# Kernel tuning notes

Hardware: AMD Instinct MI355X
Metric: run time of the kernel (lower is better)

The kernel has to match this reference:

```python
import jax, jax.numpy as jnp
import numpy as np

N_NODES = 100000


def _graph_conv(x, src, dst, W, b):
    # DGL GraphConv, norm='both':
    # out = D_in^{-1/2} A D_out^{-1/2} x W + b, degrees clamped >= 1
    ones = jnp.ones(src.shape[0], dtype=x.dtype)
    deg_out = jax.ops.segment_sum(ones, src, num_segments=N_NODES)
    deg_in = jax.ops.segment_sum(ones, dst, num_segments=N_NODES)
    norm_src = jax.lax.rsqrt(jnp.maximum(deg_out, 1.0))  # [N]
    norm_dst = jax.lax.rsqrt(jnp.maximum(deg_in, 1.0))   # [N]
    h = x * norm_src[:, None]                    # [N, d_in]
    msg = h[src]                                 # [E, d_in] gather
    agg = jax.ops.segment_sum(msg, dst, num_segments=N_NODES)  # [N, d_in] scatter-add
    agg = agg * norm_dst[:, None]
    return agg @ W + b                           # [N, d_out]


def setup_inputs() -> dict:
    key = jax.random.key(0)
    k1, k2, k3, k4, k5 = jax.random.split(key, 5)
    n_edges = 1600000
    ndim, hdl, r = 32, 64, 32
    x = jax.random.normal(k1, (N_NODES, ndim), dtype=jnp.float32)
    src = jax.random.randint(k2, (n_edges,), 0, N_NODES, dtype=jnp.int32)
    dst = jax.random.randint(k3, (n_edges,), 0, N_NODES, dtype=jnp.int32)
    W1 = jax.random.normal(k4, (ndim, hdl), dtype=jnp.float32) / np.sqrt(ndim)
    b1 = jnp.zeros((hdl,), dtype=jnp.float32)
    W2 = jax.random.normal(k5, (hdl, r), dtype=jnp.float32) / np.sqrt(hdl)
    b2 = jnp.zeros((r,), dtype=jnp.float32)
    return {"x": x, "src": src, "dst": dst, "W1": W1, "b1": b1, "W2": W2, "b2": b2}


def reference(x, src, dst, W1, b1, W2, b2):
    z = _graph_conv(x, src, dst, W1, b1)
    z = _graph_conv(z, src, dst, W2, b2)
    return z
```

## Files before the change

### kernel.cpp

```cpp
#include <hip/hip_runtime.h>

#define N_NODES 100000
#define D_IN 32
#define D_HID 64
#define D_OUT 32
#define NBUCK 391
#define CHUNK 8192
#define CAP   8192

typedef unsigned short ushort8v __attribute__((ext_vector_type(8)));
typedef unsigned short ushort4v __attribute__((ext_vector_type(4)));

__device__ __forceinline__ float bf2f(unsigned short u) {
    return __uint_as_float((unsigned)u << 16);
}
__device__ __forceinline__ unsigned short f2bf(float f) {
    unsigned u = __float_as_uint(f);
    return (unsigned short)((u + 0x7FFF + ((u >> 16) & 1)) >> 16);
}

#define REDH(a) { a += __shfl_xor(a, 4); a += __shfl_xor(a, 8); a += __shfl_xor(a, 16); }

__global__ __launch_bounds__(256) void bucket_hist_kernel(
    const int* __restrict__ src, const int* __restrict__ dst,
    int* __restrict__ sb_cnt, int* __restrict__ db_cnt, int E) {
    __shared__ int hs[NBUCK], hd[NBUCK];
    int tid = threadIdx.x;
    for (int i = tid; i < NBUCK; i += 256) { hs[i] = 0; hd[i] = 0; }
    __syncthreads();
    int stride = gridDim.x * 256;
    for (int e = blockIdx.x * 256 + tid; e < E; e += stride) {
        atomicAdd(&hs[src[e] >> 8], 1);
        atomicAdd(&hd[dst[e] >> 8], 1);
    }
    __syncthreads();
    for (int i = tid; i < NBUCK; i += 256) {
        if (hs[i]) atomicAdd(&sb_cnt[i], hs[i]);
        if (hd[i]) atomicAdd(&db_cnt[i], hd[i]);
    }
}

__global__ __launch_bounds__(512) void bucket_scan_kernel(
    const int* __restrict__ sb_cnt, const int* __restrict__ db_cnt,
    int* __restrict__ sb_base, int* __restrict__ db_base,
    int* __restrict__ sb_cur, int* __restrict__ db_cur, int E) {
    __shared__ int s[512];
    int tid = threadIdx.x;
    int v = (tid < NBUCK) ? sb_cnt[tid] : 0;
    s[tid] = v;
    __syncthreads();
    for (int off = 1; off < 512; off <<= 1) {
        int tv = (tid >= off) ? s[tid - off] : 0;
        __syncthreads(); s[tid] += tv; __syncthreads();
    }
    if (tid < NBUCK) { int e0 = s[tid] - v; sb_base[tid] = e0; sb_cur[tid] = e0; }
    if (tid == 0) sb_base[NBUCK] = E;
    __syncthreads();
    int v2 = (tid < NBUCK) ? db_cnt[tid] : 0;
    s[tid] = v2;
    __syncthreads();
    for (int off = 1; off < 512; off <<= 1) {
        int tv = (tid >= off) ? s[tid - off] : 0;
        __syncthreads(); s[tid] += tv; __syncthreads();
    }
    if (tid < NBUCK) { int e0 = s[tid] - v2; db_base[tid] = e0; db_cur[tid] = e0; }
    if (tid == 0) db_base[NBUCK] = E;
}

__global__ __launch_bounds__(512) void partition_both_kernel(
    const int* __restrict__ src, const int* __restrict__ dst,
    int* __restrict__ sb_cur, int* __restrict__ db_cur,
    int* __restrict__ ebuf, unsigned char* __restrict__ sbuf, int E) {
    __shared__ int dh[NBUCK], sh_[NBUCK];
    __shared__ int sarr[512];
    __shared__ int dloff[NBUCK], dgb[NBUCK], dcur[NBUCK];
    __shared__ int sloff[NBUCK], sgb[NBUCK], scur[NBUCK];
    __shared__ int dbuf[CHUNK];
    __shared__ unsigned char sbytes[CHUNK];
    int tid = threadIdx.x;
    int base = blockIdx.x * CHUNK;
    int lim = E - base; if (lim > CHUNK) lim = CHUNK;

    for (int i = tid; i < NBUCK; i += 512) { dh[i] = 0; sh_[i] = 0; }
    __syncthreads();
    for (int k = tid; k < lim; k += 512) {
        atomicAdd(&dh[dst[base + k] >> 8], 1);
        atomicAdd(&sh_[src[base + k] >> 8], 1);
    }
    __syncthreads();
    int v = (tid < NBUCK) ? dh[tid] : 0;
    sarr[tid] = v;
    __syncthreads();
    for (int off = 1; off < 512; off <<= 1) {
        int tv = (tid >= off) ? sarr[tid - off] : 0;
        __syncthreads(); sarr[tid] += tv; __syncthreads();
    }
    if (tid < NBUCK) {
        int excl = sarr[tid] - v;
        dloff[tid] = excl; dcur[tid] = excl;
        dgb[tid] = v ? atomicAdd(&db_cur[tid], v) : 0;
    }
    __syncthreads();
    int v2 = (tid < NBUCK) ? sh_[tid] : 0;
    sarr[tid] = v2;
    __syncthreads();
    for (int off = 1; off < 512; off <<= 1) {
        int tv = (tid >= off) ? sarr[tid - off] : 0;
        __syncthreads(); sarr[tid] += tv; __syncthreads();
    }
    if (tid < NBUCK) {
        int excl = sarr[tid] - v2;
        sloff[tid] = excl; scur[tid] = excl;
        sgb[tid] = v2 ? atomicAdd(&sb_cur[tid], v2) : 0;
    }
    __syncthreads();
    for (int k = tid; k < lim; k += 512) {
        int d = dst[base + k], s0 = src[base + k];
        int p = atomicAdd(&dcur[d >> 8], 1);
        dbuf[p] = (s0 << 8) | (d & 255);
        int p2 = atomicAdd(&scur[s0 >> 8], 1);
        sbytes[p2] = (unsigned char)(s0 & 255);
    }
    __syncthreads();
    int w = tid >> 6, lane = tid & 63;
    for (int b = w; b < NBUCK; b += 8) {
        int st = dloff[b], len = dh[b], gb = dgb[b];
        for (int i = lane; i < len; i += 64) ebuf[gb + i] = dbuf[st + i];
        int st2 = sloff[b], len2 = sh_[b], gb2 = sgb[b];
        for (int i = lane; i < len2; i += 64) sbuf[gb2 + i] = sbytes[st2 + i];
    }
}

__global__ __launch_bounds__(256) void src_norm_prescale_kernel(
    const unsigned char* __restrict__ sbuf, const int* __restrict__ sb_base,
    const float4* __restrict__ x4, ushort4v* __restrict__ xs4b,
    float* __restrict__ norm_src, int n_nodes) {
    __shared__ int cnt[256];
    __shared__ float nsl[256];
    int b = blockIdx.x, tid = threadIdx.x;
    int st = sb_base[b], en = sb_base[b + 1];
    cnt[tid] = 0;
    __syncthreads();
    for (int k = st + tid; k < en; k += 256) atomicAdd(&cnt[sbuf[k]], 1);
    __syncthreads();
    int base_node = b << 8;
    int nn = n_nodes - base_node; if (nn > 256) nn = 256;
    if (tid < nn) {
        int d = cnt[tid];
        float ns = rsqrtf((float)(d < 1 ? 1 : d));
        norm_src[base_node + tid] = ns;
        nsl[tid] = ns;
    }
    __syncthreads();
    for (int k = tid; k < nn * 8; k += 256) {
        float4 v = x4[((long)base_node << 3) + k];
        float s = nsl[k >> 3];
        ushort4v o;
        o[0] = f2bf(v.x * s); o[1] = f2bf(v.y * s);
        o[2] = f2bf(v.z * s); o[3] = f2bf(v.w * s);
        xs4b[((long)base_node << 3) + k] = o;
    }
}

__global__ __launch_bounds__(256) void localfill_kernel(
    const int* __restrict__ ebuf, const int* __restrict__ db_base,
    int* __restrict__ rowptr, float* __restrict__ norm_dst,
    int* __restrict__ colidx, int n_nodes, int E) {
    __shared__ int limg[CAP];
    __shared__ int cnt[256];
    __shared__ int sc[256];
    int b = blockIdx.x, tid = threadIdx.x;
    int base_node = b << 8;
    int nn = n_nodes - base_node; if (nn > 256) nn = 256;
    int cbase = db_base[b], cend = db_base[b + 1];
    int len = cend - cbase;
    cnt[tid] = 0;
    __syncthreads();
    for (int k = tid; k < len; k += 256) atomicAdd(&cnt[ebuf[cbase + k] & 255], 1);
    __syncthreads();
    int v = cnt[tid];
    sc[tid] = v;
    __syncthreads();
    for (int off = 1; off < 256; off <<= 1) {
        int tv = (tid >= off) ? sc[tid - off] : 0;
        __syncthreads(); sc[tid] += tv; __syncthreads();
    }
    int excl = sc[tid] - v;
    if (tid < nn) {
        rowptr[base_node + tid] = cbase + excl;
        norm_dst[base_node + tid] = rsqrtf((float)(v < 1 ? 1 : v));
    }
    if (b == NBUCK - 1 && tid == 0) rowptr[n_nodes] = E;
    __syncthreads();
    cnt[tid] = excl;
    __syncthreads();
    if (len <= CAP) {
        for (int k = tid; k < len; k += 256) {
            int v2 = ebuf[cbase + k];
            int p = atomicAdd(&cnt[v2 & 255], 1);
            limg[p] = v2 >> 8;
        }
        __syncthreads();
        for (int k = tid; k < len; k += 256) colidx[cbase + k] = limg[k];
    } else {
        for (int k = tid; k < len; k += 256) {
            int v2 = ebuf[cbase + k];
            int p = atomicAdd(&cnt[v2 & 255], 1);
            colidx[cbase + p] = v2 >> 8;
        }
    }
}

__global__ __launch_bounds__(256) void gather1_kernel(
    const ushort8v* __restrict__ xs8, const int* __restrict__ colidx,
    const int* __restrict__ rowptr, float* __restrict__ agg, int n_nodes) {
    int t = threadIdx.x;
    int w = t >> 6, lane = t & 63;
    int half = lane >> 5, hl = lane & 31;
    int eh = hl >> 2, q = hl & 3;
    int hb = half << 5;
    int npairs = (n_nodes + 1) >> 1;

    for (int p = blockIdx.x * 4 + w; p < npairs; p += gridDim.x * 4) {
        int nA = 2 * p, nB = nA + 1;
        bool hasB = nB < n_nodes;
        int rA = rowptr[nA], rA1 = rowptr[nA + 1];
        int rB1 = hasB ? rowptr[nB + 1] : rA1;
        int dA = rA1 - rA, dB = rB1 - rA1;
        int dmax = dA > dB ? dA : dB;
        int myS = half ? rA1 : rA;
        int myD = half ? dB : dA;
        float a[8];
#pragma unroll
        for (int r = 0; r < 8; ++r) a[r] = 0.f;
        for (int base = 0; base < dmax; base += 32) {
            int mylim = myD - base; mylim = mylim < 0 ? 0 : (mylim > 32 ? 32 : mylim);
            int c_reg = (hl < mylim) ? colidx[myS + base + hl] : 0;
            int c0 = __shfl(c_reg, hb | eh);
            int c1 = __shfl(c_reg, hb | (eh + 8));
            int c2 = __shfl(c_reg, hb | (eh + 16));
            int c3 = __shfl(c_reg, hb | (eh + 24));
            ushort8v v0 = xs8[(long)c0 * 4 + q];
            ushort8v v1 = xs8[(long)c1 * 4 + q];
            ushort8v v2 = xs8[(long)c2 * 4 + q];
            ushort8v v3 = xs8[(long)c3 * 4 + q];
            float m0 = (eh      < mylim) ? 1.f : 0.f;
            float m1 = (eh +  8 < mylim) ? 1.f : 0.f;
            float m2 = (eh + 16 < mylim) ? 1.f : 0.f;
            float m3 = (eh + 24 < mylim) ? 1.f : 0.f;
#pragma unroll
            for (int r = 0; r < 8; ++r) {
                a[r] = fmaf(bf2f(v0[r]), m0, a[r]);
                a[r] = fmaf(bf2f(v1[r]), m1, a[r]);
                a[r] = fmaf(bf2f(v2[r]), m2, a[r]);
                a[r] = fmaf(bf2f(v3[r]), m3, a[r]);
            }
        }
#pragma unroll
        for (int r = 0; r < 8; ++r) REDH(a[r])
        if (hl < 4) {
            int n_ = half ? nB : nA;
            if (!half || hasB) {
                float* orow = agg + (long)n_ * 32 + q * 8;
                float4 o1, o2;
                o1.x = a[0]; o1.y = a[1]; o1.z = a[2]; o1.w = a[3];
                o2.x = a[4]; o2.y = a[5]; o2.z = a[6]; o2.w = a[7];
                ((float4*)orow)[0] = o1;
                ((float4*)orow)[1] = o2;
            }
        }
    }
}

__global__ __launch_bounds__(256) void gemm_fused_kernel(
    const float* __restrict__ agg, const float* __restrict__ norm_src,
    const float* __restrict__ norm_dst,
    const float* __restrict__ W1, const float* __restrict__ b1,
    const float* __restrict__ W2, unsigned short* __restrict__ ybf, int n_nodes) {
    __shared__ float W1s[D_IN * D_HID];
    __shared__ float W2s[D_HID * D_OUT];
    __shared__ float b1s[D_HID];
    __shared__ float accs[4][2][D_IN];
    __shared__ float z1s[4][2][D_HID];
    int t = threadIdx.x;
    for (int i = t; i < 2048; i += 256) { W1s[i] = W1[i]; W2s[i] = W2[i]; }
    if (t < D_HID) b1s[t] = b1[t];
    __syncthreads();
    int w = t >> 6, lane = t & 63;
    int half = lane >> 5, hl = lane & 31;
    int npairs = (n_nodes + 1) >> 1;
    for (int p = blockIdx.x * 4 + w; p < npairs; p += gridDim.x * 4) {
        int nA = 2 * p, nB = nA + 1;
        bool hasB = nB < n_nodes;
        int nh = half ? (hasB ? nB : nA) : nA;
        accs[w][half][hl] = agg[(long)nh * 32 + hl];
        float ndA = norm_dst[nA], ndB = hasB ? norm_dst[nB] : 0.f;
        float s1A = 0.f, s1B = 0.f;
#pragma unroll
        for (int k = 0; k < D_IN; ++k) {
            float wv = W1s[k * D_HID + lane];
            s1A = fmaf(accs[w][0][k], wv, s1A);
            s1B = fmaf(accs[w][1][k], wv, s1B);
        }
        z1s[w][0][lane] = ndA * s1A + b1s[lane];
        z1s[w][1][lane] = ndB * s1B + b1s[lane];
        float s2 = 0.f;
#pragma unroll
        for (int k = 0; k < D_HID; ++k) s2 = fmaf(z1s[w][half][k], W2s[k * D_OUT + hl], s2);
        int n_ = half ? nB : nA;
        if (!half || hasB) ybf[(long)n_ * 32 + hl] = f2bf(norm_src[n_] * s2);
    }
}

__global__ __launch_bounds__(256) void gather2_kernel(
    const ushort8v* __restrict__ y8, const int* __restrict__ colidx,
    const int* __restrict__ rowptr, const float* __restrict__ norm_dst,
    const float* __restrict__ b2, float* __restrict__ out, int n_nodes) {
    int t = threadIdx.x;
    int w = t >> 6, lane = t & 63;
    int half = lane >> 5, hl = lane & 31;
    int eh = hl >> 2, q = hl & 3;
    int hb = half << 5;
    int npairs = (n_nodes + 1) >> 1;

    for (int p = blockIdx.x * 4 + w; p < npairs; p += gridDim.x * 4) {
        int nA = 2 * p, nB = nA + 1;
        bool hasB = nB < n_nodes;
        int rA = rowptr[nA], rA1 = rowptr[nA + 1];
        int rB1 = hasB ? rowptr[nB + 1] : rA1;
        int dA = rA1 - rA, dB = rB1 - rA1;
        int dmax = dA > dB ? dA : dB;
        int myS = half ? rA1 : rA;
        int myD = half ? dB : dA;
        float a[8];
#pragma unroll
        for (int r = 0; r < 8; ++r) a[r] = 0.f;
        for (int base = 0; base < dmax; base += 32) {
            int mylim = myD - base; mylim = mylim < 0 ? 0 : (mylim > 32 ? 32 : mylim);
            int c_reg = (hl < mylim) ? colidx[myS + base + hl] : 0;
            int c0 = __shfl(c_reg, hb | eh);
            int c1 = __shfl(c_reg, hb | (eh + 8));
            int c2 = __shfl(c_reg, hb | (eh + 16));
            int c3 = __shfl(c_reg, hb | (eh + 24));
            ushort8v v0 = y8[(long)c0 * 4 + q];
            ushort8v v1 = y8[(long)c1 * 4 + q];
            ushort8v v2 = y8[(long)c2 * 4 + q];
            ushort8v v3 = y8[(long)c3 * 4 + q];
            float m0 = (eh      < mylim) ? 1.f : 0.f;
            float m1 = (eh +  8 < mylim) ? 1.f : 0.f;
            float m2 = (eh + 16 < mylim) ? 1.f : 0.f;
            float m3 = (eh + 24 < mylim) ? 1.f : 0.f;
#pragma unroll
            for (int r = 0; r < 8; ++r) {
                a[r] = fmaf(bf2f(v0[r]), m0, a[r]);
                a[r] = fmaf(bf2f(v1[r]), m1, a[r]);
                a[r] = fmaf(bf2f(v2[r]), m2, a[r]);
                a[r] = fmaf(bf2f(v3[r]), m3, a[r]);
            }
        }
#pragma unroll
        for (int r = 0; r < 8; ++r) REDH(a[r])
        if (hl < 4) {
            int n_ = half ? nB : nA;
            if (!half || hasB) {
                float nd = norm_dst[n_];
                const float4 bL = ((const float4*)b2)[q * 2];
                const float4 bH = ((const float4*)b2)[q * 2 + 1];
                float4 o1, o2;
                o1.x = fmaf(a[0], nd, bL.x); o1.y = fmaf(a[1], nd, bL.y);
                o1.z = fmaf(a[2], nd, bL.z); o1.w = fmaf(a[3], nd, bL.w);
                o2.x = fmaf(a[4], nd, bH.x); o2.y = fmaf(a[5], nd, bH.y);
                o2.z = fmaf(a[6], nd, bH.z); o2.w = fmaf(a[7], nd, bH.w);
                float* orow = out + (long)n_ * 32 + q * 8;
                ((float4*)orow)[0] = o1;
                ((float4*)orow)[1] = o2;
            }
        }
    }
}

extern "C" void kernel_launch(void* const* d_in, const int* in_sizes, int n_in,
                              void* d_out, int out_size, void* d_ws, size_t ws_size,
                              hipStream_t stream) {
    const float* x   = (const float*)d_in[0];
    const int*   src = (const int*)d_in[1];
    const int*   dst = (const int*)d_in[2];
    const float* W1  = (const float*)d_in[3];
    const float* b1  = (const float*)d_in[4];
    const float* W2  = (const float*)d_in[5];
    const float* b2  = (const float*)d_in[6];

    const int N = N_NODES;
    const int E = in_sizes[1];

    int* ws_i    = (int*)d_ws;
    int* sb_cnt  = ws_i;
    int* db_cnt  = ws_i + 512;
    int* sb_base = ws_i + 1024;
    int* db_base = ws_i + 1536;
    int* sb_cur  = ws_i + 2048;
    int* db_cur  = ws_i + 2560;
    int* rowptr  = ws_i + 3072;
    int* colidx  = ws_i + 103104;
    float* norms = (float*)(ws_i + 1703104);
    int* ebuf    = ws_i + 1903104;
    unsigned char* sbuf = (unsigned char*)(ws_i + 3503104);
    unsigned short* xsb = (unsigned short*)(ws_i + 3903104);
    float* agg   = (float*)(ws_i + 5503104);
    unsigned short* ybf = (unsigned short*)ebuf;

    hipMemsetAsync(ws_i, 0, 1024 * sizeof(int), stream);

    bucket_hist_kernel<<<256, 256, 0, stream>>>(src, dst, sb_cnt, db_cnt, E);
    bucket_scan_kernel<<<1, 512, 0, stream>>>(sb_cnt, db_cnt, sb_base, db_base,
                                              sb_cur, db_cur, E);

    int pb = (E + CHUNK - 1) / CHUNK;
    partition_both_kernel<<<pb, 512, 0, stream>>>(src, dst, sb_cur, db_cur,
                                                  ebuf, sbuf, E);
    src_norm_prescale_kernel<<<NBUCK, 256, 0, stream>>>(sbuf, sb_base,
                                                        (const float4*)x, (ushort4v*)xsb,
                                                        norms, N);
    localfill_kernel<<<NBUCK, 256, 0, stream>>>(ebuf, db_base, rowptr, norms + N,
                                                colidx, N, E);

    gather1_kernel<<<2048, 256, 0, stream>>>((const ushort8v*)xsb, colidx, rowptr,
                                             agg, N);
    gemm_fused_kernel<<<2048, 256, 0, stream>>>(agg, norms, norms + N,
                                                W1, b1, W2, ybf, N);
    gather2_kernel<<<2048, 256, 0, stream>>>((const ushort8v*)ybf, colidx, rowptr,
                                             norms + N, b2, (float*)d_out, N);
}
```

Baseline: 175.0 us.

## Merge bucket finalize kernels, use quarter-wave per node in gathers, replace memset

The source-norm prescale and the CSR localfill kernels are merged into one per-bucket kernel, which removes a launch and its dependency gap. Both gather kernels now give each 16-lane quarter-wave one destination node instead of each 32-lane half-wave, so a wave processes four nodes. Average in-degree is about 16, so less of each wave sits idle on masked lanes. The memset is replaced by a tiny zeroing kernel to avoid memset API overhead. The merged kernel uses more shared memory per block, and the quarter-wave layout needs more loop iterations for high-degree nodes.

```diff
diff --git a/kernel.cpp b/kernel.cpp
--- a/kernel.cpp
+++ b/kernel.cpp
@@ -19,7 +19,9 @@
     return (unsigned short)((u + 0x7FFF + ((u >> 16) & 1)) >> 16);
 }
 
-#define REDH(a) { a += __shfl_xor(a, 4); a += __shfl_xor(a, 8); a += __shfl_xor(a, 16); }
+__global__ void zero_counts_kernel(int* __restrict__ p) {
+    p[blockIdx.x * 256 + threadIdx.x] = 0;
+}
 
 __global__ __launch_bounds__(256) void bucket_hist_kernel(
     const int* __restrict__ src, const int* __restrict__ dst,
@@ -131,20 +133,26 @@
     }
 }
 
-__global__ __launch_bounds__(256) void src_norm_prescale_kernel(
+__global__ __launch_bounds__(256) void bucket_finalize_kernel(
     const unsigned char* __restrict__ sbuf, const int* __restrict__ sb_base,
     const float4* __restrict__ x4, ushort4v* __restrict__ xs4b,
-    float* __restrict__ norm_src, int n_nodes) {
+    float* __restrict__ norm_src,
+    const int* __restrict__ ebuf, const int* __restrict__ db_base,
+    int* __restrict__ rowptr, float* __restrict__ norm_dst,
+    int* __restrict__ colidx, int n_nodes, int E) {
+    __shared__ int limg[CAP];
     __shared__ int cnt[256];
+    __shared__ int sc[256];
     __shared__ float nsl[256];
     int b = blockIdx.x, tid = threadIdx.x;
+    int base_node = b << 8;
+    int nn = n_nodes - base_node; if (nn > 256) nn = 256;
+
     int st = sb_base[b], en = sb_base[b + 1];
     cnt[tid] = 0;
     __syncthreads();
     for (int k = st + tid; k < en; k += 256) atomicAdd(&cnt[sbuf[k]], 1);
     __syncthreads();
-    int base_node = b << 8;
-    int nn = n_nodes - base_node; if (nn > 256) nn = 256;
     if (tid < nn) {
         int d = cnt[tid];
         float ns = rsqrtf((float)(d < 1 ? 1 : d));
@@ -160,20 +168,10 @@
         o[2] = f2bf(v.z * s); o[3] = f2bf(v.w * s);
         xs4b[((long)base_node << 3) + k] = o;
     }
-}
-
-__global__ __launch_bounds__(256) void localfill_kernel(
-    const int* __restrict__ ebuf, const int* __restrict__ db_base,
-    int* __restrict__ rowptr, float* __restrict__ norm_dst,
-    int* __restrict__ colidx, int n_nodes, int E) {
-    __shared__ int limg[CAP];
-    __shared__ int cnt[256];
-    __shared__ int sc[256];
-    int b = blockIdx.x, tid = threadIdx.x;
-    int base_node = b << 8;
-    int nn = n_nodes - base_node; if (nn > 256) nn = 256;
+
     int cbase = db_base[b], cend = db_base[b + 1];
     int len = cend - cbase;
+    __syncthreads();
     cnt[tid] = 0;
     __syncthreads();
     for (int k = tid; k < len; k += 256) atomicAdd(&cnt[ebuf[cbase + k] & 255], 1);
@@ -216,38 +214,40 @@
     const int* __restrict__ rowptr, float* __restrict__ agg, int n_nodes) {
     int t = threadIdx.x;
     int w = t >> 6, lane = t & 63;
-    int half = lane >> 5, hl = lane & 31;
-    int eh = hl >> 2, q = hl & 3;
-    int hb = half << 5;
-    int npairs = (n_nodes + 1) >> 1;
-
-    for (int p = blockIdx.x * 4 + w; p < npairs; p += gridDim.x * 4) {
-        int nA = 2 * p, nB = nA + 1;
-        bool hasB = nB < n_nodes;
-        int rA = rowptr[nA], rA1 = rowptr[nA + 1];
-        int rB1 = hasB ? rowptr[nB + 1] : rA1;
-        int dA = rA1 - rA, dB = rB1 - rA1;
-        int dmax = dA > dB ? dA : dB;
-        int myS = half ? rA1 : rA;
-        int myD = half ? dB : dA;
+    int quarter = lane >> 4, ql = lane & 15;
+    int eh = ql >> 2, q = ql & 3;
+    int qb = quarter << 4;
+    int nquads = (n_nodes + 3) >> 2;
+
+    for (int p = blockIdx.x * 4 + w; p < nquads; p += gridDim.x * 4) {
+        int base_node = p << 2;
+        int idx = base_node + lane;
+        if (idx > n_nodes) idx = n_nodes;
+        int rr = (lane < 5) ? rowptr[idx] : 0;
+        int myS = __shfl(rr, quarter);
+        int myE = __shfl(rr, quarter + 1);
+        int myD = myE - myS;
+        int dm = myD;
+        dm = max(dm, __shfl_xor(dm, 16));
+        dm = max(dm, __shfl_xor(dm, 32));
         float a[8];
 #pragma unroll
         for (int r = 0; r < 8; ++r) a[r] = 0.f;
-        for (int base = 0; base < dmax; base += 32) {
-            int mylim = myD - base; mylim = mylim < 0 ? 0 : (mylim > 32 ? 32 : mylim);
-            int c_reg = (hl < mylim) ? colidx[myS + base + hl] : 0;
-            int c0 = __shfl(c_reg, hb | eh);
-            int c1 = __shfl(c_reg, hb | (eh + 8));
-            int c2 = __shfl(c_reg, hb | (eh + 16));
-            int c3 = __shfl(c_reg, hb | (eh + 24));
+        for (int base = 0; base < dm; base += 16) {
+            int mylim = myD - base; mylim = mylim < 0 ? 0 : (mylim > 16 ? 16 : mylim);
+            int c_reg = (ql < mylim) ? colidx[myS + base + ql] : 0;
+            int c0 = __shfl(c_reg, qb | eh);
+            int c1 = __shfl(c_reg, qb | (eh + 4));
+            int c2 = __shfl(c_reg, qb | (eh + 8));
+            int c3 = __shfl(c_reg, qb | (eh + 12));
             ushort8v v0 = xs8[(long)c0 * 4 + q];
             ushort8v v1 = xs8[(long)c1 * 4 + q];
             ushort8v v2 = xs8[(long)c2 * 4 + q];
             ushort8v v3 = xs8[(long)c3 * 4 + q];
             float m0 = (eh      < mylim) ? 1.f : 0.f;
-            float m1 = (eh +  8 < mylim) ? 1.f : 0.f;
-            float m2 = (eh + 16 < mylim) ? 1.f : 0.f;
-            float m3 = (eh + 24 < mylim) ? 1.f : 0.f;
+            float m1 = (eh +  4 < mylim) ? 1.f : 0.f;
+            float m2 = (eh +  8 < mylim) ? 1.f : 0.f;
+            float m3 = (eh + 12 < mylim) ? 1.f : 0.f;
 #pragma unroll
             for (int r = 0; r < 8; ++r) {
                 a[r] = fmaf(bf2f(v0[r]), m0, a[r]);
@@ -257,11 +257,11 @@
             }
         }
 #pragma unroll
-        for (int r = 0; r < 8; ++r) REDH(a[r])
-        if (hl < 4) {
-            int n_ = half ? nB : nA;
-            if (!half || hasB) {
-                float* orow = agg + (long)n_ * 32 + q * 8;
+        for (int r = 0; r < 8; ++r) { a[r] += __shfl_xor(a[r], 4); a[r] += __shfl_xor(a[r], 8); }
+        if (ql < 4) {
+            int n_ = base_node + quarter;
+            if (n_ < n_nodes) {
+                float* orow = agg + (long)n_ * 32 + ql * 8;
                 float4 o1, o2;
                 o1.x = a[0]; o1.y = a[1]; o1.z = a[2]; o1.w = a[3];
                 o2.x = a[4]; o2.y = a[5]; o2.z = a[6]; o2.w = a[7];
@@ -318,38 +318,40 @@
     const float* __restrict__ b2, float* __restrict__ out, int n_nodes) {
     int t = threadIdx.x;
     int w = t >> 6, lane = t & 63;
-    int half = lane >> 5, hl = lane & 31;
-    int eh = hl >> 2, q = hl & 3;
-    int hb = half << 5;
-    int npairs = (n_nodes + 1) >> 1;
-
-    for (int p = blockIdx.x * 4 + w; p < npairs; p += gridDim.x * 4) {
-        int nA = 2 * p, nB = nA + 1;
-        bool hasB = nB < n_nodes;
-        int rA = rowptr[nA], rA1 = rowptr[nA + 1];
-        int rB1 = hasB ? rowptr[nB + 1] : rA1;
-        int dA = rA1 - rA, dB = rB1 - rA1;
-        int dmax = dA > dB ? dA : dB;
-        int myS = half ? rA1 : rA;
-        int myD = half ? dB : dA;
+    int quarter = lane >> 4, ql = lane & 15;
+    int eh = ql >> 2, q = ql & 3;
+    int qb = quarter << 4;
+    int nquads = (n_nodes + 3) >> 2;
+
+    for (int p = blockIdx.x * 4 + w; p < nquads; p += gridDim.x * 4) {
+        int base_node = p << 2;
+        int idx = base_node + lane;
+        if (idx > n_nodes) idx = n_nodes;
+        int rr = (lane < 5) ? rowptr[idx] : 0;
+        int myS = __shfl(rr, quarter);
+        int myE = __shfl(rr, quarter + 1);
+        int myD = myE - myS;
+        int dm = myD;
+        dm = max(dm, __shfl_xor(dm, 16));
+        dm = max(dm, __shfl_xor(dm, 32));
         float a[8];
 #pragma unroll
         for (int r = 0; r < 8; ++r) a[r] = 0.f;
-        for (int base = 0; base < dmax; base += 32) {
-            int mylim = myD - base; mylim = mylim < 0 ? 0 : (mylim > 32 ? 32 : mylim);
-            int c_reg = (hl < mylim) ? colidx[myS + base + hl] : 0;
-            int c0 = __shfl(c_reg, hb | eh);
-            int c1 = __shfl(c_reg, hb | (eh + 8));
-            int c2 = __shfl(c_reg, hb | (eh + 16));
-            int c3 = __shfl(c_reg, hb | (eh + 24));
+        for (int base = 0; base < dm; base += 16) {
+            int mylim = myD - base; mylim = mylim < 0 ? 0 : (mylim > 16 ? 16 : mylim);
+            int c_reg = (ql < mylim) ? colidx[myS + base + ql] : 0;
+            int c0 = __shfl(c_reg, qb | eh);
+            int c1 = __shfl(c_reg, qb | (eh + 4));
+            int c2 = __shfl(c_reg, qb | (eh + 8));
+            int c3 = __shfl(c_reg, qb | (eh + 12));
             ushort8v v0 = y8[(long)c0 * 4 + q];
             ushort8v v1 = y8[(long)c1 * 4 + q];
             ushort8v v2 = y8[(long)c2 * 4 + q];
             ushort8v v3 = y8[(long)c3 * 4 + q];
             float m0 = (eh      < mylim) ? 1.f : 0.f;
-            float m1 = (eh +  8 < mylim) ? 1.f : 0.f;
-            float m2 = (eh + 16 < mylim) ? 1.f : 0.f;
-            float m3 = (eh + 24 < mylim) ? 1.f : 0.f;
+            float m1 = (eh +  4 < mylim) ? 1.f : 0.f;
+            float m2 = (eh +  8 < mylim) ? 1.f : 0.f;
+            float m3 = (eh + 12 < mylim) ? 1.f : 0.f;
 #pragma unroll
             for (int r = 0; r < 8; ++r) {
                 a[r] = fmaf(bf2f(v0[r]), m0, a[r]);
@@ -359,19 +361,19 @@
             }
         }
 #pragma unroll
-        for (int r = 0; r < 8; ++r) REDH(a[r])
-        if (hl < 4) {
-            int n_ = half ? nB : nA;
-            if (!half || hasB) {
+        for (int r = 0; r < 8; ++r) { a[r] += __shfl_xor(a[r], 4); a[r] += __shfl_xor(a[r], 8); }
+        if (ql < 4) {
+            int n_ = base_node + quarter;
+            if (n_ < n_nodes) {
                 float nd = norm_dst[n_];
-                const float4 bL = ((const float4*)b2)[q * 2];
-                const float4 bH = ((const float4*)b2)[q * 2 + 1];
+                const float4 bL = ((const float4*)b2)[ql * 2];
+                const float4 bH = ((const float4*)b2)[ql * 2 + 1];
                 float4 o1, o2;
                 o1.x = fmaf(a[0], nd, bL.x); o1.y = fmaf(a[1], nd, bL.y);
                 o1.z = fmaf(a[2], nd, bL.z); o1.w = fmaf(a[3], nd, bL.w);
                 o2.x = fmaf(a[4], nd, bH.x); o2.y = fmaf(a[5], nd, bH.y);
                 o2.z = fmaf(a[6], nd, bH.z); o2.w = fmaf(a[7], nd, bH.w);
-                float* orow = out + (long)n_ * 32 + q * 8;
+                float* orow = out + (long)n_ * 32 + ql * 8;
                 ((float4*)orow)[0] = o1;
                 ((float4*)orow)[1] = o2;
             }
@@ -409,7 +411,7 @@
     float* agg   = (float*)(ws_i + 5503104);
     unsigned short* ybf = (unsigned short*)ebuf;
 
-    hipMemsetAsync(ws_i, 0, 1024 * sizeof(int), stream);
+    zero_counts_kernel<<<4, 256, 0, stream>>>(ws_i);
 
     bucket_hist_kernel<<<256, 256, 0, stream>>>(src, dst, sb_cnt, db_cnt, E);
     bucket_scan_kernel<<<1, 512, 0, stream>>>(sb_cnt, db_cnt, sb_base, db_base,
@@ -418,11 +420,10 @@
     int pb = (E + CHUNK - 1) / CHUNK;
     partition_both_kernel<<<pb, 512, 0, stream>>>(src, dst, sb_cur, db_cur,
                                                   ebuf, sbuf, E);
-    src_norm_prescale_kernel<<<NBUCK, 256, 0, stream>>>(sbuf, sb_base,
-                                                        (const float4*)x, (ushort4v*)xsb,
-                                                        norms, N);
-    localfill_kernel<<<NBUCK, 256, 0, stream>>>(ebuf, db_base, rowptr, norms + N,
-                                                colidx, N, E);
+    bucket_finalize_kernel<<<NBUCK, 256, 0, stream>>>(sbuf, sb_base,
+                                                      (const float4*)x, (ushort4v*)xsb,
+                                                      norms, ebuf, db_base, rowptr,
+                                                      norms + N, colidx, N, E);
 
     gather1_kernel<<<2048, 256, 0, stream>>>((const ushort8v*)xsb, colidx, rowptr,
                                              agg, N);
```

Result: faster. 163.2 us, median of 2 (-6.7%).
